# Optimization experiments

Hardware: AMD Instinct MI355X
Metric: run time of the kernel (lower is better)

## Reference

```python
import jax, jax.numpy as jnp
import numpy as np

B, N, D = 8, 1024, 768
H = 12
HD = D // H  # 64
SCALE = HD ** (-0.5)


def setup_inputs() -> dict:
    key = jax.random.key(0)
    ks = jax.random.split(key, 11)
    s = 0.02
    return {
        "x": jax.random.normal(ks[0], (B, N, D), dtype=jnp.float32),
        "w_q": jax.random.normal(ks[1], (D, D), dtype=jnp.float32) * s,
        "b_q": jax.random.normal(ks[2], (D,), dtype=jnp.float32) * s,
        "w_k": jax.random.normal(ks[3], (D, D), dtype=jnp.float32) * s,
        "b_k": jax.random.normal(ks[4], (D,), dtype=jnp.float32) * s,
        "w_v": jax.random.normal(ks[5], (D, D), dtype=jnp.float32) * s,
        "b_v": jax.random.normal(ks[6], (D,), dtype=jnp.float32) * s,
        "w_qt": jax.random.normal(ks[7], (D, D), dtype=jnp.float32) * s,
        "b_qt": jax.random.normal(ks[8], (D,), dtype=jnp.float32) * s,
        "w_p": jax.random.normal(ks[9], (D, D), dtype=jnp.float32) * s,
        "b_p": jax.random.normal(ks[10], (D,), dtype=jnp.float32) * s,
    }


def _heads(y):
    # [B,N,D] -> [B,H,N,HD]
    b, n, d = y.shape
    return y.reshape(b, n, H, HD).transpose(0, 2, 1, 3)


def reference(x, w_q, b_q, w_k, b_k, w_v, b_v, w_qt, b_qt, w_p, b_p):
    # torch nn.Linear: y = x @ W.T + b
    q = _heads(x @ w_q.T + b_q)
    k = _heads(x @ w_k.T + b_k)
    v = _heads(x @ w_v.T + b_v)
    q_tilde = _heads(x @ w_qt.T + b_qt)
    # NOTE: source divides by self.scale = head_dim**-0.5 (i.e. multiplies by sqrt(hd)); reproduced faithfully
    corr = jnp.einsum("bhnd,bhmd->bhnm", q_tilde, k) / SCALE
    scores = jnp.einsum("bhnd,bhmd->bhnm", q, k) / SCALE + corr
    attn = jax.nn.softmax(scores, axis=-1)
    out = jnp.einsum("bhnm,bhmd->bhnd", attn, v)  # [B,H,N,HD]
    out = out.transpose(0, 2, 1, 3).reshape(x.shape[0], x.shape[1], D)
    out = out @ w_p.T + b_p
    return out, corr
```

## Files before the change

### kernel.cpp

```cpp
#include <hip/hip_runtime.h>

typedef __bf16 bf16_t;
typedef __bf16 bf16x8 __attribute__((ext_vector_type(8)));
typedef __bf16 bf16x4 __attribute__((ext_vector_type(4)));
typedef float f32x4 __attribute__((ext_vector_type(4)));

constexpr int BATCH = 8;
constexpr int NSEQ = 1024;
constexpr int DMODEL = 768;
constexpr int NH = 12;
constexpr int HDIM = 64;
constexpr int MROWS = BATCH * NSEQ;
constexpr int WSZ = DMODEL * DMODEL;
constexpr float L2E = 1.44269504088896f;

#define AS1(p) ((const __attribute__((address_space(1))) void*)(p))
#define AS3(p) ((__attribute__((address_space(3))) void*)(p))

__global__ __launch_bounds__(256) void prep_w(
    const float* __restrict__ wq, const float* __restrict__ wqt,
    const float* __restrict__ wk, const float* __restrict__ wv,
    const float* __restrict__ wp, const float* __restrict__ bq,
    const float* __restrict__ bqt, ushort* __restrict__ wb_,
    float* __restrict__ bqs, float* __restrict__ bqt8)
{
    int i = blockIdx.x * 256 + threadIdx.x;
    bf16_t* w = (bf16_t*)wb_;
    float a = wq[i], b = wqt[i];
    w[i]            = (bf16_t)(8.0f * (a + b));
    w[WSZ + i]      = (bf16_t)(8.0f * b);
    w[2*WSZ + i]    = (bf16_t)wk[i];
    w[3*WSZ + i]    = (bf16_t)wv[i];
    w[4*WSZ + i]    = (bf16_t)wp[i];
    if (i < DMODEL) {
        bqs[i]  = 8.0f * (bq[i] + bqt[i]);
        bqt8[i] = 8.0f * bqt[i];
    }
}

__global__ __launch_bounds__(256) void conv_x(const float* __restrict__ x,
                                              ushort* __restrict__ xb_)
{
    int i = (blockIdx.x * 256 + threadIdx.x) * 4;
    float4 v = *(const float4*)(x + i);
    bf16x4 r = { (bf16_t)v.x, (bf16_t)v.y, (bf16_t)v.z, (bf16_t)v.w };
    *(bf16x4*)((bf16_t*)xb_ + i) = r;
}

__device__ __forceinline__ void gemm_core(
    const bf16_t* __restrict__ A, const bf16_t* __restrict__ W,
    bf16_t* As, bf16_t* Bs, int m0, int n0, int tid, f32x4 acc[4][4])
{
    const int lane = tid & 63, wave = tid >> 6;
    const int g = lane >> 4, c = lane & 15;
    const int wm = wave >> 1, wn = wave & 1;

    const int r_b = tid >> 3;
    const int koff = 8 * ((tid & 7) ^ (r_b & 7));
    const size_t arow = (size_t)(m0 + r_b) * DMODEL + koff;
    const size_t brow = (size_t)(n0 + r_b) * DMODEL + koff;
    char* As_base = (char*)As + (tid & ~63) * 16;
    char* Bs_base = (char*)Bs + (tid & ~63) * 16;

    for (int k0 = 0; k0 < DMODEL; k0 += 64) {
        __syncthreads();
#pragma unroll
        for (int i = 0; i < 4; i++)
            __builtin_amdgcn_global_load_lds(
                AS1(A + arow + k0 + (size_t)i * 32 * DMODEL),
                AS3(As_base + i * 4096), 16, 0, 0);
#pragma unroll
        for (int i = 0; i < 4; i++)
            __builtin_amdgcn_global_load_lds(
                AS1(W + brow + k0 + (size_t)i * 32 * DMODEL),
                AS3(Bs_base + i * 4096), 16, 0, 0);
        __syncthreads();
#pragma unroll
        for (int kk = 0; kk < 2; kk++) {
            bf16x8 af[4], bfr[4];
#pragma unroll
            for (int mt = 0; mt < 4; mt++) {
                int r = wm * 64 + mt * 16 + c;
                af[mt] = *(const bf16x8*)(As + r * 64 + ((kk * 4 + g) ^ (r & 7)) * 8);
            }
#pragma unroll
            for (int nt = 0; nt < 4; nt++) {
                int r = wn * 64 + nt * 16 + c;
                bfr[nt] = *(const bf16x8*)(Bs + r * 64 + ((kk * 4 + g) ^ (r & 7)) * 8);
            }
#pragma unroll
            for (int mt = 0; mt < 4; mt++)
#pragma unroll
                for (int nt = 0; nt < 4; nt++)
                    acc[mt][nt] = __builtin_amdgcn_mfma_f32_16x16x32_bf16(
                        af[mt], bfr[nt], acc[mt][nt], 0, 0, 0);
        }
    }
}

__global__ __launch_bounds__(256) void gemm_qkv(
    const ushort* __restrict__ xb_, const ushort* __restrict__ wb_,
    const float* __restrict__ bqs, const float* __restrict__ bqt8,
    const float* __restrict__ bk, const float* __restrict__ bv,
    ushort* __restrict__ o0, ushort* __restrict__ o1,
    ushort* __restrict__ o2, ushort* __restrict__ o3)
{
    __shared__ alignas(16) bf16_t As[128 * 64];
    __shared__ alignas(16) bf16_t Bs[128 * 64];
    const int bid = blockIdx.x;
    const int gid = (bid & 7) * 192 + (bid >> 3);
    const int z = gid / 384;
    const int rr = gid % 384;
    const int m0 = (rr / 6) * 128, n0 = (rr % 6) * 128;

    const bf16_t* A = (const bf16_t*)xb_;
    const bf16_t* W = (const bf16_t*)wb_ + (size_t)z * WSZ;
    const float* bias = (z == 0) ? bqs : (z == 1) ? bqt8 : (z == 2) ? bk : bv;
    bf16_t* outp = (bf16_t*)((z == 0) ? o0 : (z == 1) ? o1 : (z == 2) ? o2 : o3);
    f32x4 acc[4][4] = {};
    gemm_core(A, W, As, Bs, m0, n0, threadIdx.x, acc);

    const int tid = threadIdx.x, lane = tid & 63, wave = tid >> 6;
    const int g = lane >> 4, c = lane & 15;
    const int wm = wave >> 1, wn = wave & 1;
#pragma unroll
    for (int mt = 0; mt < 4; mt++)
#pragma unroll
        for (int nt = 0; nt < 4; nt++) {
            int col = n0 + wn * 64 + nt * 16 + c;
            int h = col >> 6, hd = col & 63;
            float bsv = bias[col];
#pragma unroll
            for (int j = 0; j < 4; j++) {
                int row = m0 + wm * 64 + mt * 16 + 4 * g + j;
                int b = row >> 10, ns = row & 1023;
                outp[(((size_t)b * NH + h) * NSEQ + ns) * HDIM + hd] =
                    (bf16_t)(acc[mt][nt][j] + bsv);
            }
        }
}

__global__ __launch_bounds__(256) void gemm_out(
    const ushort* __restrict__ ao_, const ushort* __restrict__ wp_,
    const float* __restrict__ bp, float* __restrict__ out)
{
    __shared__ alignas(16) bf16_t As[128 * 64];
    __shared__ alignas(16) bf16_t Bs[128 * 64];
    const int bid = blockIdx.x;
    const int gid = (bid & 7) * 48 + (bid >> 3);
    const int m0 = (gid / 6) * 128, n0 = (gid % 6) * 128;

    const bf16_t* A = (const bf16_t*)ao_;
    const bf16_t* W = (const bf16_t*)wp_;
    f32x4 acc[4][4] = {};
    gemm_core(A, W, As, Bs, m0, n0, threadIdx.x, acc);

    const int tid = threadIdx.x, lane = tid & 63, wave = tid >> 6;
    const int g = lane >> 4, c = lane & 15;
    const int wm = wave >> 1, wn = wave & 1;
#pragma unroll
    for (int mt = 0; mt < 4; mt++)
#pragma unroll
        for (int nt = 0; nt < 4; nt++) {
            int col = n0 + wn * 64 + nt * 16 + c;
            float bsv = bp[col];
#pragma unroll
            for (int j = 0; j < 4; j++) {
                int row = m0 + wm * 64 + mt * 16 + 4 * g + j;
                out[(size_t)row * DMODEL + col] = acc[mt][nt][j] + bsv;
            }
        }
}

__global__ __launch_bounds__(256, 2) void attn_kernel(
    const ushort* __restrict__ qs_, const ushort* __restrict__ qt_,
    const ushort* __restrict__ kb_, const ushort* __restrict__ vb_,
    ushort* __restrict__ ao_, float* __restrict__ corr)
{
    __shared__ alignas(16) bf16_t VT[2][64 * 64];
    __shared__ alignas(16) bf16_t P[4][32 * 72];
    const bf16_t* QS = (const bf16_t*)qs_;
    const bf16_t* QT = (const bf16_t*)qt_;
    const bf16_t* Kb = (const bf16_t*)kb_;
    const bf16_t* Vb = (const bf16_t*)vb_;
    bf16_t* Ob = (bf16_t*)ao_;

    const int tid = threadIdx.x;
    const int w = tid >> 6, lane = tid & 63;
    const int g = lane >> 4, c = lane & 15;
    const int bid = blockIdx.x;
    const int gid = (bid & 7) * 96 + (bid >> 3);
    const int bh = gid >> 3, qb = gid & 7;
    const int q00 = qb * 128 + w * 32;
    const size_t base = (size_t)bh * (NSEQ * HDIM);

    bf16x8 qsf[2][2], qtf[2][2];
#pragma unroll
    for (int s = 0; s < 2; s++)
#pragma unroll
        for (int kk = 0; kk < 2; kk++) {
            const size_t qrow = base + (size_t)(q00 + s * 16 + c) * HDIM + kk * 32 + 8 * g;
            qsf[s][kk] = *(const bf16x8*)(QS + qrow);
            qtf[s][kk] = *(const bf16x8*)(QT + qrow);
        }
    f32x4 oacc[2][4] = {};
    float mrun[2], lrun[2];
#pragma unroll
    for (int s = 0; s < 2; s++) { mrun[s] = -3e30f; lrun[s] = 0.f; }

    float* corr_b = corr + (size_t)bh * (NSEQ * NSEQ);

    for (int t = 0; t < 16; t++) {
        const int kv0 = t * 64;
        bf16_t* vt = VT[t & 1];
#pragma unroll
        for (int r2 = 0; r2 < 2; r2++) {
            const int hd0 = (r2 * 4 + w) * 8;
            bf16x8 vv = *(const bf16x8*)(Vb + base + (size_t)(kv0 + lane) * HDIM + hd0);
#pragma unroll
            for (int e = 0; e < 8; e++) {
                const int hd = hd0 + e;
                vt[hd * 64 + (lane ^ ((hd & 7) << 3))] = vv[e];
            }
        }
        bf16x8 kf[4][2];
#pragma unroll
        for (int kvt = 0; kvt < 4; kvt++) {
            const size_t krow = base + (size_t)(kv0 + kvt * 16 + c) * HDIM + 8 * g;
            kf[kvt][0] = *(const bf16x8*)(Kb + krow);
            kf[kvt][1] = *(const bf16x8*)(Kb + krow + 32);
        }
        f32x4 sv[2][4];
#pragma unroll
        for (int kvt = 0; kvt < 4; kvt++) {
#pragma unroll
            for (int s = 0; s < 2; s++) {
                f32x4 sa = {0.f, 0.f, 0.f, 0.f};
                f32x4 ca = {0.f, 0.f, 0.f, 0.f};
                sa = __builtin_amdgcn_mfma_f32_16x16x32_bf16(kf[kvt][0], qsf[s][0], sa, 0, 0, 0);
                sa = __builtin_amdgcn_mfma_f32_16x16x32_bf16(kf[kvt][1], qsf[s][1], sa, 0, 0, 0);
                ca = __builtin_amdgcn_mfma_f32_16x16x32_bf16(kf[kvt][0], qtf[s][0], ca, 0, 0, 0);
                ca = __builtin_amdgcn_mfma_f32_16x16x32_bf16(kf[kvt][1], qtf[s][1], ca, 0, 0, 0);
                sv[s][kvt] = sa;
                *(f32x4*)(corr_b + (size_t)(q00 + s * 16 + c) * NSEQ + kv0 + kvt * 16 + 4 * g) = ca;
            }
        }
#pragma unroll
        for (int s = 0; s < 2; s++) {
            f32x4 mm;
#pragma unroll
            for (int j = 0; j < 4; j++)
                mm[j] = fmaxf(fmaxf(sv[s][0][j], sv[s][1][j]),
                              fmaxf(sv[s][2][j], sv[s][3][j]));
            float tm = fmaxf(fmaxf(mm[0], mm[1]), fmaxf(mm[2], mm[3]));
            tm = fmaxf(tm, __shfl_xor(tm, 16));
            tm = fmaxf(tm, __shfl_xor(tm, 32));
            if (__any(tm > mrun[s] + 8.0f)) {
                float newm = fmaxf(mrun[s], tm);
                float scl = exp2f((mrun[s] - newm) * L2E);
                mrun[s] = newm;
                lrun[s] *= scl;
#pragma unroll
                for (int j = 0; j < 4; j++) {
                    float scj = __shfl(scl, 4 * g + j);
#pragma unroll
                    for (int nt = 0; nt < 4; nt++) oacc[s][nt][j] *= scj;
                }
            }
            const float mneg = mrun[s] * L2E;
            float ps = 0.f;
#pragma unroll
            for (int kvt = 0; kvt < 4; kvt++)
#pragma unroll
                for (int j = 0; j < 4; j++) {
                    float p = exp2f(__builtin_fmaf(sv[s][kvt][j], L2E, -mneg));
                    sv[s][kvt][j] = p;
                    ps += p;
                }
            ps += __shfl_xor(ps, 16);
            ps += __shfl_xor(ps, 32);
            lrun[s] += ps;
#pragma unroll
            for (int kvt = 0; kvt < 4; kvt++) {
                bf16x4 pb = { (bf16_t)sv[s][kvt][0], (bf16_t)sv[s][kvt][1],
                              (bf16_t)sv[s][kvt][2], (bf16_t)sv[s][kvt][3] };
                *(bf16x4*)(&P[w][(s * 16 + c) * 72 + kvt * 16 + 4 * g]) = pb;
            }
        }
        asm volatile("s_waitcnt lgkmcnt(0)" ::: "memory");
        __builtin_amdgcn_sched_barrier(0);
        __builtin_amdgcn_s_barrier();
#pragma unroll
        for (int kk = 0; kk < 2; kk++) {
#pragma unroll
            for (int nt = 0; nt < 4; nt++) {
                const int hd = nt * 16 + c;
                bf16x8 vf = *(const bf16x8*)(&vt[hd * 64 + ((kk * 32 + 8 * g) ^ ((hd & 7) << 3))]);
#pragma unroll
                for (int s = 0; s < 2; s++) {
                    bf16x8 pa = *(const bf16x8*)(&P[w][(s * 16 + c) * 72 + kk * 32 + 8 * g]);
                    oacc[s][nt] = __builtin_amdgcn_mfma_f32_16x16x32_bf16(pa, vf, oacc[s][nt], 0, 0, 0);
                }
            }
        }
    }
    const int b = bh / NH, h = bh % NH;
#pragma unroll
    for (int s = 0; s < 2; s++) {
        float lj[4];
#pragma unroll
        for (int j = 0; j < 4; j++) lj[j] = __shfl(lrun[s], 4 * g + j);
#pragma unroll
        for (int nt = 0; nt < 4; nt++)
#pragma unroll
            for (int j = 0; j < 4; j++) {
                float val = oacc[s][nt][j] / lj[j];
                Ob[(size_t)(b * NSEQ + q00 + s * 16 + 4 * g + j) * DMODEL + h * HDIM + nt * 16 + c] =
                    (bf16_t)val;
            }
    }
}

extern "C" void kernel_launch(void* const* d_in, const int* in_sizes, int n_in,
                              void* d_out, int out_size, void* d_ws, size_t ws_size,
                              hipStream_t stream)
{
    const float* x   = (const float*)d_in[0];
    const float* wq  = (const float*)d_in[1];
    const float* bq  = (const float*)d_in[2];
    const float* wk  = (const float*)d_in[3];
    const float* bk  = (const float*)d_in[4];
    const float* wv  = (const float*)d_in[5];
    const float* bv  = (const float*)d_in[6];
    const float* wqt = (const float*)d_in[7];
    const float* bqt = (const float*)d_in[8];
    const float* wp  = (const float*)d_in[9];
    const float* bp  = (const float*)d_in[10];

    char* ws = (char*)d_ws;
    ushort* xb   = (ushort*)(ws);
    ushort* wb   = (ushort*)(ws + 12582912);
    float*  bqs  = (float*)(ws + 18481152);
    float*  bqt8 = (float*)(ws + 18485248);
    ushort* qs   = (ushort*)(ws + 18489344);
    ushort* qt   = qs + 6291456;
    ushort* kb   = qt + 6291456;
    ushort* vb   = kb + 6291456;
    ushort* ao   = vb + 6291456;

    float* out  = (float*)d_out;
    float* corr = out + (size_t)6291456;

    prep_w<<<2304, 256, 0, stream>>>(wq, wqt, wk, wv, wp, bq, bqt, wb, bqs, bqt8);
    conv_x<<<6144, 256, 0, stream>>>(x, xb);
    gemm_qkv<<<1536, 256, 0, stream>>>(xb, wb, bqs, bqt8, bk, bv, qs, qt, kb, vb);
    attn_kernel<<<768, 256, 0, stream>>>(qs, qt, kb, vb, ao, corr);
    gemm_out<<<384, 256, 0, stream>>>(ao, wb + (size_t)4 * WSZ, bp, out);
}
```

Baseline: 245.3 us.

## Store V pre-transposed from QKV GEMM to skip per-tile transpose in attention

The QKV projection epilogue now writes V in [B,H,HD,N] layout with 4-wide bf16 vector stores, instead of [B,H,N,HD]. The attention kernel then loads V tiles already transposed as 16-byte vectors and stores them to LDS with a chunk-level XOR swizzle. This replaces the per-element scalar LDS scatter used for the transpose. The cost is a different global write pattern in the GEMM epilogue for V, and the design change spans two kernels.

```diff
diff --git a/kernel.cpp b/kernel.cpp
--- a/kernel.cpp
+++ b/kernel.cpp
@@ -130,12 +130,22 @@
             int col = n0 + wn * 64 + nt * 16 + c;
             int h = col >> 6, hd = col & 63;
             float bsv = bias[col];
-#pragma unroll
-            for (int j = 0; j < 4; j++) {
-                int row = m0 + wm * 64 + mt * 16 + 4 * g + j;
-                int b = row >> 10, ns = row & 1023;
-                outp[(((size_t)b * NH + h) * NSEQ + ns) * HDIM + hd] =
-                    (bf16_t)(acc[mt][nt][j] + bsv);
+            if (z == 3) {
+                int row0 = m0 + wm * 64 + mt * 16 + 4 * g;
+                int b = row0 >> 10, ns0 = row0 & 1023;
+                bf16x4 pb = { (bf16_t)(acc[mt][nt][0] + bsv),
+                              (bf16_t)(acc[mt][nt][1] + bsv),
+                              (bf16_t)(acc[mt][nt][2] + bsv),
+                              (bf16_t)(acc[mt][nt][3] + bsv) };
+                *(bf16x4*)(outp + ((size_t)(b * NH + h) * HDIM + hd) * NSEQ + ns0) = pb;
+            } else {
+#pragma unroll
+                for (int j = 0; j < 4; j++) {
+                    int row = m0 + wm * 64 + mt * 16 + 4 * g + j;
+                    int b = row >> 10, ns = row & 1023;
+                    outp[(((size_t)b * NH + h) * NSEQ + ns) * HDIM + hd] =
+                        (bf16_t)(acc[mt][nt][j] + bsv);
+                }
             }
         }
 }
@@ -174,7 +184,7 @@
 
 __global__ __launch_bounds__(256, 2) void attn_kernel(
     const ushort* __restrict__ qs_, const ushort* __restrict__ qt_,
-    const ushort* __restrict__ kb_, const ushort* __restrict__ vb_,
+    const ushort* __restrict__ kb_, const ushort* __restrict__ vt_,
     ushort* __restrict__ ao_, float* __restrict__ corr)
 {
     __shared__ alignas(16) bf16_t VT[2][64 * 64];
@@ -182,7 +192,7 @@
     const bf16_t* QS = (const bf16_t*)qs_;
     const bf16_t* QT = (const bf16_t*)qt_;
     const bf16_t* Kb = (const bf16_t*)kb_;
-    const bf16_t* Vb = (const bf16_t*)vb_;
+    const bf16_t* Vt = (const bf16_t*)vt_;
     bf16_t* Ob = (bf16_t*)ao_;
 
     const int tid = threadIdx.x;
@@ -210,18 +220,17 @@
 
     float* corr_b = corr + (size_t)bh * (NSEQ * NSEQ);
 
+    const int hd0_ = tid >> 3, ch0_ = tid & 7;
+    const int hd1_ = hd0_ + 32;
+
     for (int t = 0; t < 16; t++) {
         const int kv0 = t * 64;
         bf16_t* vt = VT[t & 1];
-#pragma unroll
-        for (int r2 = 0; r2 < 2; r2++) {
-            const int hd0 = (r2 * 4 + w) * 8;
-            bf16x8 vv = *(const bf16x8*)(Vb + base + (size_t)(kv0 + lane) * HDIM + hd0);
-#pragma unroll
-            for (int e = 0; e < 8; e++) {
-                const int hd = hd0 + e;
-                vt[hd * 64 + (lane ^ ((hd & 7) << 3))] = vv[e];
-            }
+        {
+            bf16x8 v0 = *(const bf16x8*)(Vt + base + (size_t)hd0_ * NSEQ + kv0 + ch0_ * 8);
+            bf16x8 v1 = *(const bf16x8*)(Vt + base + (size_t)hd1_ * NSEQ + kv0 + ch0_ * 8);
+            *(bf16x8*)(vt + hd0_ * 64 + ((ch0_ ^ (hd0_ & 7)) * 8)) = v0;
+            *(bf16x8*)(vt + hd1_ * 64 + ((ch0_ ^ (hd1_ & 7)) * 8)) = v1;
         }
         bf16x8 kf[4][2];
 #pragma unroll
@@ -295,7 +304,7 @@
 #pragma unroll
             for (int nt = 0; nt < 4; nt++) {
                 const int hd = nt * 16 + c;
-                bf16x8 vf = *(const bf16x8*)(&vt[hd * 64 + ((kk * 32 + 8 * g) ^ ((hd & 7) << 3))]);
+                bf16x8 vf = *(const bf16x8*)(&vt[hd * 64 + (((kk * 4 + g) ^ (hd & 7)) * 8)]);
 #pragma unroll
                 for (int s = 0; s < 2; s++) {
                     bf16x8 pa = *(const bf16x8*)(&P[w][(s * 16 + c) * 72 + kk * 32 + 8 * g]);
@@ -345,15 +354,15 @@
     ushort* qs   = (ushort*)(ws + 18489344);
     ushort* qt   = qs + 6291456;
     ushort* kb   = qt + 6291456;
-    ushort* vb   = kb + 6291456;
-    ushort* ao   = vb + 6291456;
+    ushort* vt   = kb + 6291456;
+    ushort* ao   = vt + 6291456;
 
     float* out  = (float*)d_out;
     float* corr = out + (size_t)6291456;
 
     prep_w<<<2304, 256, 0, stream>>>(wq, wqt, wk, wv, wp, bq, bqt, wb, bqs, bqt8);
     conv_x<<<6144, 256, 0, stream>>>(x, xb);
-    gemm_qkv<<<1536, 256, 0, stream>>>(xb, wb, bqs, bqt8, bk, bv, qs, qt, kb, vb);
-    attn_kernel<<<768, 256, 0, stream>>>(qs, qt, kb, vb, ao, corr);
+    gemm_qkv<<<1536, 256, 0, stream>>>(xb, wb, bqs, bqt8, bk, bv, qs, qt, kb, vt);
+    attn_kernel<<<768, 256, 0, stream>>>(qs, qt, kb, vt, ao, corr);
     gemm_out<<<384, 256, 0, stream>>>(ao, wb + (size_t)4 * WSZ, bp, out);
 }
```

Result: no change. 248.3 us (+1.2%).
